# Optimization experiments

Measured on AMD Instinct MI355X. Metric: run time of the kernel, lower is better.

The kernel has to match this reference:

```python
import jax, jax.numpy as jnp
import numpy as np

DELTA = 0.1      # delta from __init__
LN_EPS = 1e-5    # torch LayerNorm default eps

B, IN, OUT, E = 256, 512, 512, 256


def setup_inputs() -> dict:
    key = jax.random.key(0)
    ks = jax.random.split(key, 6)
    return {
        "x": jax.random.normal(ks[0], (B, IN), dtype=jnp.float32),
        # nn.init.normal_(std=0.1), shape (out_features, in_features)
        "weights": 0.1 * jax.random.normal(ks[1], (OUT, IN), dtype=jnp.float32),
        # frozen predicate embeddings (in_features, embedding_dim)
        "pred_emb": jax.random.normal(ks[2], (IN, E), dtype=jnp.float32),
        # nn.Linear(E, OUT): weight (OUT, E), bias (OUT,)
        "attn_w": jax.random.uniform(ks[3], (OUT, E), dtype=jnp.float32,
                                      minval=-1.0, maxval=1.0) / np.sqrt(E),
        "attn_b": jax.random.uniform(ks[4], (OUT,), dtype=jnp.float32,
                                      minval=-1.0, maxval=1.0) / np.sqrt(E),
        # nn.LayerNorm(OUT)
        "ln_g": jnp.ones((OUT,), dtype=jnp.float32),
        "ln_b": jnp.zeros((OUT,), dtype=jnp.float32),
    }


def _layernorm(s, g, b):
    mu = s.mean(axis=-1, keepdims=True)
    var = ((s - mu) ** 2).mean(axis=-1, keepdims=True)
    return (s - mu) * jax.lax.rsqrt(var + LN_EPS) * g + b


def reference(x, weights, pred_emb, attn_w, attn_b, ln_g, ln_b):
    # semantic attention gate: batch-invariant, compute once -> (IN, OUT)
    scores = pred_emb @ attn_w.T + attn_b                    # (IN, OUT)
    sig = jax.nn.sigmoid(_layernorm(scores, ln_g, ln_b))     # (IN, OUT)

    xe = x[:, :, None]                                       # (B, IN, 1)
    wt = weights.T[None]                                     # (1, IN, OUT)
    # abs_weight * attn_adjusted, fused elementwise -> (B, IN, OUT)
    aw = jnp.abs(xe * wt) * (sig[None] * xe)

    bias = aw.max(axis=1) - aw.sum(axis=1)                   # CONJUNCTION: max - sum
    return x @ weights.T + DELTA * bias                      # (B, OUT)
```

## Files before the change

kernel.cpp:

```cpp
#include <hip/hip_runtime.h>
#include <hip/hip_bf16.h>
#include <math.h>

#define B_   256
#define IN_  512
#define OUT_ 512
#define E_   256
#define DELTA_ 0.1f
#define LN_EPS_ 1e-5f

__global__ __launch_bounds__(512)
void k1_scores_ln_sig(const float* __restrict__ pred_emb,
                      const float* __restrict__ attn_w,
                      const float* __restrict__ attn_b,
                      const float* __restrict__ ln_g,
                      const float* __restrict__ ln_b,
                      const float* __restrict__ weights,
                      float2* __restrict__ wv) {
    __shared__ float pe[2][E_];
    __shared__ float red[8][2][2];
    __shared__ float smu[2], srs[2];

    const int t    = threadIdx.x;
    const int lane = t & 63;
    const int wid  = t >> 6;
    const int i0   = blockIdx.x * 2;
    const int o    = t;

    pe[t >> 8][t & 255] = pred_emb[(size_t)(i0 + (t >> 8)) * E_ + (t & 255)];
    __syncthreads();

    const float4* p0 = reinterpret_cast<const float4*>(pe[0]);
    const float4* p1 = reinterpret_cast<const float4*>(pe[1]);
    const float4* wrow = reinterpret_cast<const float4*>(attn_w + (size_t)o * E_);

    float a0 = 0.f, a1 = 0.f;
    #pragma unroll 8
    for (int e4 = 0; e4 < E_ / 4; ++e4) {
        float4 w4 = wrow[e4];
        float4 q0 = p0[e4];
        float4 q1 = p1[e4];
        a0 += q0.x * w4.x + q0.y * w4.y + q0.z * w4.z + q0.w * w4.w;
        a1 += q1.x * w4.x + q1.y * w4.y + q1.z * w4.z + q1.w * w4.w;
    }
    const float bo = attn_b[o];
    a0 += bo;
    a1 += bo;

    {
        float s1 = a0, s2 = a0 * a0;
        float u1 = a1, u2 = a1 * a1;
        #pragma unroll
        for (int off = 32; off > 0; off >>= 1) {
            s1 += __shfl_down(s1, off);
            s2 += __shfl_down(s2, off);
            u1 += __shfl_down(u1, off);
            u2 += __shfl_down(u2, off);
        }
        if (lane == 0) {
            red[wid][0][0] = s1; red[wid][0][1] = s2;
            red[wid][1][0] = u1; red[wid][1][1] = u2;
        }
    }
    __syncthreads();
    if (t < 2) {
        float s1 = 0.f, s2 = 0.f;
        #pragma unroll
        for (int w = 0; w < 8; ++w) { s1 += red[w][t][0]; s2 += red[w][t][1]; }
        float mu  = s1 / (float)OUT_;
        float var = s2 / (float)OUT_ - mu * mu;
        smu[t] = mu;
        srs[t] = rsqrtf(var + LN_EPS_);
    }
    __syncthreads();

    const float g  = ln_g[o];
    const float bb = ln_b[o];
    float z0 = (a0 - smu[0]) * srs[0] * g + bb;
    float z1 = (a1 - smu[1]) * srs[1] * g + bb;
    float sg0 = 1.f / (1.f + expf(-z0));
    float sg1 = 1.f / (1.f + expf(-z1));

    float2 w01 = *reinterpret_cast<const float2*>(weights + (size_t)o * IN_ + i0);
    wv[(size_t)(i0 + 0) * OUT_ + o] = make_float2(w01.x, fabsf(w01.x) * sg0);
    wv[(size_t)(i0 + 1) * OUT_ + o] = make_float2(w01.y, fabsf(w01.y) * sg1);
}

#define K2_SK 4
#define K2_CH 128
#define K2_BO (B_ * OUT_)

__global__ __launch_bounds__(256)
void k2_partials(const float* __restrict__ x,
                 const float2* __restrict__ wv,
                 float* __restrict__ plin,
                 float* __restrict__ pmax) {
    __shared__ float4 xs4[64 * 33];
    __shared__ float2 ws2[K2_CH * 17];

    const int t  = threadIdx.x;
    const int ot = t & 15;
    const int bl = t >> 4;
    const int o0 = blockIdx.x * 16;
    const int b0 = blockIdx.y * 64;
    const int sk = blockIdx.z;
    const int i0 = sk * K2_CH;

    #pragma unroll
    for (int k = 0; k < 8; ++k) {
        int p    = t + k * 256;
        int row  = p >> 5;
        int col4 = p & 31;
        xs4[row * 33 + col4] = reinterpret_cast<const float4*>(
            x + (size_t)(b0 + row) * IN_ + i0)[col4];
    }
    #pragma unroll
    for (int k = 0; k < 8; ++k) {
        int r = bl + 16 * k;
        ws2[r * 17 + ot] = wv[(size_t)(i0 + r) * OUT_ + o0 + ot];
    }
    __syncthreads();

    const int o = o0 + ot;
    float d0 = 0.f, s0 = 0.f, m0 = -INFINITY;
    float d1 = 0.f, s1 = 0.f, m1 = -INFINITY;
    float d2 = 0.f, s2 = 0.f, m2 = -INFINITY;
    float d3 = 0.f, s3 = 0.f, m3 = -INFINITY;

    #pragma unroll 2
    for (int i4 = 0; i4 < K2_CH / 4; ++i4) {
        float4 x0 = xs4[(bl +  0) * 33 + i4];
        float4 x1 = xs4[(bl + 16) * 33 + i4];
        float4 x2 = xs4[(bl + 32) * 33 + i4];
        float4 x3 = xs4[(bl + 48) * 33 + i4];
        float2 w0 = ws2[(4 * i4 + 0) * 17 + ot];
        float2 w1 = ws2[(4 * i4 + 1) * 17 + ot];
        float2 w2 = ws2[(4 * i4 + 2) * 17 + ot];
        float2 w3 = ws2[(4 * i4 + 3) * 17 + ot];
        float p;
        float4 u0 = make_float4(x0.x * fabsf(x0.x), x0.y * fabsf(x0.y),
                                x0.z * fabsf(x0.z), x0.w * fabsf(x0.w));
        float4 u1 = make_float4(x1.x * fabsf(x1.x), x1.y * fabsf(x1.y),
                                x1.z * fabsf(x1.z), x1.w * fabsf(x1.w));
        float4 u2 = make_float4(x2.x * fabsf(x2.x), x2.y * fabsf(x2.y),
                                x2.z * fabsf(x2.z), x2.w * fabsf(x2.w));
        float4 u3 = make_float4(x3.x * fabsf(x3.x), x3.y * fabsf(x3.y),
                                x3.z * fabsf(x3.z), x3.w * fabsf(x3.w));

        d0 = fmaf(x0.x, w0.x, d0); p = u0.x * w0.y; s0 += p; m0 = fmaxf(m0, p);
        d1 = fmaf(x1.x, w0.x, d1); p = u1.x * w0.y; s1 += p; m1 = fmaxf(m1, p);
        d2 = fmaf(x2.x, w0.x, d2); p = u2.x * w0.y; s2 += p; m2 = fmaxf(m2, p);
        d3 = fmaf(x3.x, w0.x, d3); p = u3.x * w0.y; s3 += p; m3 = fmaxf(m3, p);

        d0 = fmaf(x0.y, w1.x, d0); p = u0.y * w1.y; s0 += p; m0 = fmaxf(m0, p);
        d1 = fmaf(x1.y, w1.x, d1); p = u1.y * w1.y; s1 += p; m1 = fmaxf(m1, p);
        d2 = fmaf(x2.y, w1.x, d2); p = u2.y * w1.y; s2 += p; m2 = fmaxf(m2, p);
        d3 = fmaf(x3.y, w1.x, d3); p = u3.y * w1.y; s3 += p; m3 = fmaxf(m3, p);

        d0 = fmaf(x0.z, w2.x, d0); p = u0.z * w2.y; s0 += p; m0 = fmaxf(m0, p);
        d1 = fmaf(x1.z, w2.x, d1); p = u1.z * w2.y; s1 += p; m1 = fmaxf(m1, p);
        d2 = fmaf(x2.z, w2.x, d2); p = u2.z * w2.y; s2 += p; m2 = fmaxf(m2, p);
        d3 = fmaf(x3.z, w2.x, d3); p = u3.z * w2.y; s3 += p; m3 = fmaxf(m3, p);

        d0 = fmaf(x0.w, w3.x, d0); p = u0.w * w3.y; s0 += p; m0 = fmaxf(m0, p);
        d1 = fmaf(x1.w, w3.x, d1); p = u1.w * w3.y; s1 += p; m1 = fmaxf(m1, p);
        d2 = fmaf(x2.w, w3.x, d2); p = u2.w * w3.y; s2 += p; m2 = fmaxf(m2, p);
        d3 = fmaf(x3.w, w3.x, d3); p = u3.w * w3.y; s3 += p; m3 = fmaxf(m3, p);
    }

    const size_t base = (size_t)sk * K2_BO + (size_t)b0 * OUT_ + o;
    plin[base + (size_t)(bl +  0) * OUT_] = d0 - DELTA_ * s0;
    plin[base + (size_t)(bl + 16) * OUT_] = d1 - DELTA_ * s1;
    plin[base + (size_t)(bl + 32) * OUT_] = d2 - DELTA_ * s2;
    plin[base + (size_t)(bl + 48) * OUT_] = d3 - DELTA_ * s3;
    pmax[base + (size_t)(bl +  0) * OUT_] = m0;
    pmax[base + (size_t)(bl + 16) * OUT_] = m1;
    pmax[base + (size_t)(bl + 32) * OUT_] = m2;
    pmax[base + (size_t)(bl + 48) * OUT_] = m3;
}

__global__ __launch_bounds__(256)
void k3_combine(const float4* __restrict__ plin4,
                const float4* __restrict__ pmax4,
                float4* __restrict__ out4) {
    const int g = blockIdx.x * 256 + threadIdx.x;
    const int Q = K2_BO / 4;
    float4 l0 = plin4[g], l1 = plin4[Q + g], l2 = plin4[2 * Q + g], l3 = plin4[3 * Q + g];
    float4 m0 = pmax4[g], m1 = pmax4[Q + g], m2 = pmax4[2 * Q + g], m3 = pmax4[3 * Q + g];
    float4 r;
    r.x = (l0.x + l1.x + l2.x + l3.x) + DELTA_ * fmaxf(fmaxf(m0.x, m1.x), fmaxf(m2.x, m3.x));
    r.y = (l0.y + l1.y + l2.y + l3.y) + DELTA_ * fmaxf(fmaxf(m0.y, m1.y), fmaxf(m2.y, m3.y));
    r.z = (l0.z + l1.z + l2.z + l3.z) + DELTA_ * fmaxf(fmaxf(m0.z, m1.z), fmaxf(m2.z, m3.z));
    r.w = (l0.w + l1.w + l2.w + l3.w) + DELTA_ * fmaxf(fmaxf(m0.w, m1.w), fmaxf(m2.w, m3.w));
    out4[g] = r;
}

extern "C" void kernel_launch(void* const* d_in, const int* in_sizes, int n_in,
                              void* d_out, int out_size, void* d_ws, size_t ws_size,
                              hipStream_t stream) {
    const float* x        = (const float*)d_in[0];
    const float* weights  = (const float*)d_in[1];
    const float* pred_emb = (const float*)d_in[2];
    const float* attn_w   = (const float*)d_in[3];
    const float* attn_b   = (const float*)d_in[4];
    const float* ln_g     = (const float*)d_in[5];
    const float* ln_b     = (const float*)d_in[6];

    float2* wv   = (float2*)d_ws;
    float*  plin = (float*)d_ws + 2 * (size_t)IN_ * OUT_;
    float*  pmax = plin + (size_t)K2_SK * K2_BO;

    k1_scores_ln_sig<<<IN_ / 2, 512, 0, stream>>>(
        pred_emb, attn_w, attn_b, ln_g, ln_b, weights, wv);

    k2_partials<<<dim3(OUT_ / 16, B_ / 64, K2_SK), 256, 0, stream>>>(
        x, wv, plin, pmax);

    k3_combine<<<K2_BO / 4 / 256, 256, 0, stream>>>(
        (const float4*)plin, (const float4*)pmax, (float4*)d_out);
}
```

Baseline: 99.47 us.

## Use 4x4 register tiles in partials kernel with split W/V arrays

The interleaved float2 weight/gate array is split into two planar arrays, with DELTA folded into the gate values so the combine step adds the max directly. The partials kernel now computes a 4-batch by 4-output register tile per thread from float4 shared-memory loads, with 64 outputs per block and split-K raised from 4 to 8 chunks of 64. The gate kernel handles four input rows per block. The aim is more arithmetic per shared-memory load and vectorised stores, at the cost of more registers and double the partial-buffer traffic in the combine kernel.

```diff
diff --git a/kernel.cpp b/kernel.cpp
--- a/kernel.cpp
+++ b/kernel.cpp
@@ -1,5 +1,4 @@
 #include <hip/hip_runtime.h>
-#include <hip/hip_bf16.h>
 #include <math.h>
 
 #define B_   256
@@ -16,54 +15,68 @@
                       const float* __restrict__ ln_g,
                       const float* __restrict__ ln_b,
                       const float* __restrict__ weights,
-                      float2* __restrict__ wv) {
-    __shared__ float pe[2][E_];
-    __shared__ float red[8][2][2];
-    __shared__ float smu[2], srs[2];
+                      float* __restrict__ wA,
+                      float* __restrict__ vA) {
+    __shared__ float pe[4][E_];
+    __shared__ float red[8][4][2];
+    __shared__ float smu[4], srs[4];
 
     const int t    = threadIdx.x;
     const int lane = t & 63;
     const int wid  = t >> 6;
-    const int i0   = blockIdx.x * 2;
+    const int i0   = blockIdx.x * 4;
     const int o    = t;
 
-    pe[t >> 8][t & 255] = pred_emb[(size_t)(i0 + (t >> 8)) * E_ + (t & 255)];
+    #pragma unroll
+    for (int k = 0; k < 2; ++k) {
+        int p = t + 512 * k;
+        pe[p >> 8][p & 255] = pred_emb[(size_t)(i0 + (p >> 8)) * E_ + (p & 255)];
+    }
     __syncthreads();
 
     const float4* p0 = reinterpret_cast<const float4*>(pe[0]);
     const float4* p1 = reinterpret_cast<const float4*>(pe[1]);
+    const float4* p2 = reinterpret_cast<const float4*>(pe[2]);
+    const float4* p3 = reinterpret_cast<const float4*>(pe[3]);
     const float4* wrow = reinterpret_cast<const float4*>(attn_w + (size_t)o * E_);
 
-    float a0 = 0.f, a1 = 0.f;
+    float a0 = 0.f, a1 = 0.f, a2 = 0.f, a3 = 0.f;
     #pragma unroll 8
     for (int e4 = 0; e4 < E_ / 4; ++e4) {
         float4 w4 = wrow[e4];
         float4 q0 = p0[e4];
         float4 q1 = p1[e4];
+        float4 q2 = p2[e4];
+        float4 q3 = p3[e4];
         a0 += q0.x * w4.x + q0.y * w4.y + q0.z * w4.z + q0.w * w4.w;
         a1 += q1.x * w4.x + q1.y * w4.y + q1.z * w4.z + q1.w * w4.w;
+        a2 += q2.x * w4.x + q2.y * w4.y + q2.z * w4.z + q2.w * w4.w;
+        a3 += q3.x * w4.x + q3.y * w4.y + q3.z * w4.z + q3.w * w4.w;
     }
     const float bo = attn_b[o];
-    a0 += bo;
-    a1 += bo;
+    a0 += bo; a1 += bo; a2 += bo; a3 += bo;
 
     {
-        float s1 = a0, s2 = a0 * a0;
-        float u1 = a1, u2 = a1 * a1;
+        float s10 = a0, s20 = a0 * a0;
+        float s11 = a1, s21 = a1 * a1;
+        float s12 = a2, s22 = a2 * a2;
+        float s13 = a3, s23 = a3 * a3;
         #pragma unroll
         for (int off = 32; off > 0; off >>= 1) {
-            s1 += __shfl_down(s1, off);
-            s2 += __shfl_down(s2, off);
-            u1 += __shfl_down(u1, off);
-            u2 += __shfl_down(u2, off);
+            s10 += __shfl_down(s10, off); s20 += __shfl_down(s20, off);
+            s11 += __shfl_down(s11, off); s21 += __shfl_down(s21, off);
+            s12 += __shfl_down(s12, off); s22 += __shfl_down(s22, off);
+            s13 += __shfl_down(s13, off); s23 += __shfl_down(s23, off);
         }
         if (lane == 0) {
-            red[wid][0][0] = s1; red[wid][0][1] = s2;
-            red[wid][1][0] = u1; red[wid][1][1] = u2;
-        }
-    }
-    __syncthreads();
-    if (t < 2) {
+            red[wid][0][0] = s10; red[wid][0][1] = s20;
+            red[wid][1][0] = s11; red[wid][1][1] = s21;
+            red[wid][2][0] = s12; red[wid][2][1] = s22;
+            red[wid][3][0] = s13; red[wid][3][1] = s23;
+        }
+    }
+    __syncthreads();
+    if (t < 4) {
         float s1 = 0.f, s2 = 0.f;
         #pragma unroll
         for (int w = 0; w < 8; ++w) { s1 += red[w][t][0]; s2 += red[w][t][1]; }
@@ -78,105 +91,111 @@
     const float bb = ln_b[o];
     float z0 = (a0 - smu[0]) * srs[0] * g + bb;
     float z1 = (a1 - smu[1]) * srs[1] * g + bb;
+    float z2 = (a2 - smu[2]) * srs[2] * g + bb;
+    float z3 = (a3 - smu[3]) * srs[3] * g + bb;
     float sg0 = 1.f / (1.f + expf(-z0));
     float sg1 = 1.f / (1.f + expf(-z1));
-
-    float2 w01 = *reinterpret_cast<const float2*>(weights + (size_t)o * IN_ + i0);
-    wv[(size_t)(i0 + 0) * OUT_ + o] = make_float2(w01.x, fabsf(w01.x) * sg0);
-    wv[(size_t)(i0 + 1) * OUT_ + o] = make_float2(w01.y, fabsf(w01.y) * sg1);
-}
-
-#define K2_SK 4
-#define K2_CH 128
+    float sg2 = 1.f / (1.f + expf(-z2));
+    float sg3 = 1.f / (1.f + expf(-z3));
+
+    float4 w4 = *reinterpret_cast<const float4*>(weights + (size_t)o * IN_ + i0);
+    wA[(size_t)(i0 + 0) * OUT_ + o] = w4.x;
+    wA[(size_t)(i0 + 1) * OUT_ + o] = w4.y;
+    wA[(size_t)(i0 + 2) * OUT_ + o] = w4.z;
+    wA[(size_t)(i0 + 3) * OUT_ + o] = w4.w;
+    vA[(size_t)(i0 + 0) * OUT_ + o] = DELTA_ * fabsf(w4.x) * sg0;
+    vA[(size_t)(i0 + 1) * OUT_ + o] = DELTA_ * fabsf(w4.y) * sg1;
+    vA[(size_t)(i0 + 2) * OUT_ + o] = DELTA_ * fabsf(w4.z) * sg2;
+    vA[(size_t)(i0 + 3) * OUT_ + o] = DELTA_ * fabsf(w4.w) * sg3;
+}
+
+#define K2_SK 8
+#define K2_CH 64
 #define K2_BO (B_ * OUT_)
 
 __global__ __launch_bounds__(256)
 void k2_partials(const float* __restrict__ x,
-                 const float2* __restrict__ wv,
+                 const float* __restrict__ wA,
+                 const float* __restrict__ vA,
                  float* __restrict__ plin,
                  float* __restrict__ pmax) {
-    __shared__ float4 xs4[64 * 33];
-    __shared__ float2 ws2[K2_CH * 17];
+    __shared__ float4 xs [64 * 17];
+    __shared__ float4 wss[64 * 17];
+    __shared__ float4 vss[64 * 17];
 
     const int t  = threadIdx.x;
-    const int ot = t & 15;
-    const int bl = t >> 4;
-    const int o0 = blockIdx.x * 16;
+    const int oq = t & 15;
+    const int br = t >> 4;
+    const int o0 = blockIdx.x * 64;
     const int b0 = blockIdx.y * 64;
-    const int sk = blockIdx.z;
-    const int i0 = sk * K2_CH;
-
-    #pragma unroll
-    for (int k = 0; k < 8; ++k) {
-        int p    = t + k * 256;
-        int row  = p >> 5;
-        int col4 = p & 31;
-        xs4[row * 33 + col4] = reinterpret_cast<const float4*>(
-            x + (size_t)(b0 + row) * IN_ + i0)[col4];
-    }
-    #pragma unroll
-    for (int k = 0; k < 8; ++k) {
-        int r = bl + 16 * k;
-        ws2[r * 17 + ot] = wv[(size_t)(i0 + r) * OUT_ + o0 + ot];
-    }
-    __syncthreads();
-
-    const int o = o0 + ot;
-    float d0 = 0.f, s0 = 0.f, m0 = -INFINITY;
-    float d1 = 0.f, s1 = 0.f, m1 = -INFINITY;
-    float d2 = 0.f, s2 = 0.f, m2 = -INFINITY;
-    float d3 = 0.f, s3 = 0.f, m3 = -INFINITY;
+    const int i0 = blockIdx.z * K2_CH;
+
+    #pragma unroll
+    for (int k = 0; k < 4; ++k) {
+        int p   = t + k * 256;
+        int row = p >> 4;
+        int c4  = p & 15;
+        xs [row * 17 + c4] = *reinterpret_cast<const float4*>(
+            x  + (size_t)(b0 + row) * IN_  + i0 + c4 * 4);
+        wss[row * 17 + c4] = *reinterpret_cast<const float4*>(
+            wA + (size_t)(i0 + row) * OUT_ + o0 + c4 * 4);
+        vss[row * 17 + c4] = *reinterpret_cast<const float4*>(
+            vA + (size_t)(i0 + row) * OUT_ + o0 + c4 * 4);
+    }
+    __syncthreads();
+
+    float d[4][4], s[4][4], m[4][4];
+    #pragma unroll
+    for (int b = 0; b < 4; ++b)
+        #pragma unroll
+        for (int oo = 0; oo < 4; ++oo) {
+            d[b][oo] = 0.f; s[b][oo] = 0.f; m[b][oo] = -INFINITY;
+        }
 
     #pragma unroll 2
     for (int i4 = 0; i4 < K2_CH / 4; ++i4) {
-        float4 x0 = xs4[(bl +  0) * 33 + i4];
-        float4 x1 = xs4[(bl + 16) * 33 + i4];
-        float4 x2 = xs4[(bl + 32) * 33 + i4];
-        float4 x3 = xs4[(bl + 48) * 33 + i4];
-        float2 w0 = ws2[(4 * i4 + 0) * 17 + ot];
-        float2 w1 = ws2[(4 * i4 + 1) * 17 + ot];
-        float2 w2 = ws2[(4 * i4 + 2) * 17 + ot];
-        float2 w3 = ws2[(4 * i4 + 3) * 17 + ot];
-        float p;
-        float4 u0 = make_float4(x0.x * fabsf(x0.x), x0.y * fabsf(x0.y),
-                                x0.z * fabsf(x0.z), x0.w * fabsf(x0.w));
-        float4 u1 = make_float4(x1.x * fabsf(x1.x), x1.y * fabsf(x1.y),
-                                x1.z * fabsf(x1.z), x1.w * fabsf(x1.w));
-        float4 u2 = make_float4(x2.x * fabsf(x2.x), x2.y * fabsf(x2.y),
-                                x2.z * fabsf(x2.z), x2.w * fabsf(x2.w));
-        float4 u3 = make_float4(x3.x * fabsf(x3.x), x3.y * fabsf(x3.y),
-                                x3.z * fabsf(x3.z), x3.w * fabsf(x3.w));
-
-        d0 = fmaf(x0.x, w0.x, d0); p = u0.x * w0.y; s0 += p; m0 = fmaxf(m0, p);
-        d1 = fmaf(x1.x, w0.x, d1); p = u1.x * w0.y; s1 += p; m1 = fmaxf(m1, p);
-        d2 = fmaf(x2.x, w0.x, d2); p = u2.x * w0.y; s2 += p; m2 = fmaxf(m2, p);
-        d3 = fmaf(x3.x, w0.x, d3); p = u3.x * w0.y; s3 += p; m3 = fmaxf(m3, p);
-
-        d0 = fmaf(x0.y, w1.x, d0); p = u0.y * w1.y; s0 += p; m0 = fmaxf(m0, p);
-        d1 = fmaf(x1.y, w1.x, d1); p = u1.y * w1.y; s1 += p; m1 = fmaxf(m1, p);
-        d2 = fmaf(x2.y, w1.x, d2); p = u2.y * w1.y; s2 += p; m2 = fmaxf(m2, p);
-        d3 = fmaf(x3.y, w1.x, d3); p = u3.y * w1.y; s3 += p; m3 = fmaxf(m3, p);
-
-        d0 = fmaf(x0.z, w2.x, d0); p = u0.z * w2.y; s0 += p; m0 = fmaxf(m0, p);
-        d1 = fmaf(x1.z, w2.x, d1); p = u1.z * w2.y; s1 += p; m1 = fmaxf(m1, p);
-        d2 = fmaf(x2.z, w2.x, d2); p = u2.z * w2.y; s2 += p; m2 = fmaxf(m2, p);
-        d3 = fmaf(x3.z, w2.x, d3); p = u3.z * w2.y; s3 += p; m3 = fmaxf(m3, p);
-
-        d0 = fmaf(x0.w, w3.x, d0); p = u0.w * w3.y; s0 += p; m0 = fmaxf(m0, p);
-        d1 = fmaf(x1.w, w3.x, d1); p = u1.w * w3.y; s1 += p; m1 = fmaxf(m1, p);
-        d2 = fmaf(x2.w, w3.x, d2); p = u2.w * w3.y; s2 += p; m2 = fmaxf(m2, p);
-        d3 = fmaf(x3.w, w3.x, d3); p = u3.w * w3.y; s3 += p; m3 = fmaxf(m3, p);
-    }
-
-    const size_t base = (size_t)sk * K2_BO + (size_t)b0 * OUT_ + o;
-    plin[base + (size_t)(bl +  0) * OUT_] = d0 - DELTA_ * s0;
-    plin[base + (size_t)(bl + 16) * OUT_] = d1 - DELTA_ * s1;
-    plin[base + (size_t)(bl + 32) * OUT_] = d2 - DELTA_ * s2;
-    plin[base + (size_t)(bl + 48) * OUT_] = d3 - DELTA_ * s3;
-    pmax[base + (size_t)(bl +  0) * OUT_] = m0;
-    pmax[base + (size_t)(bl + 16) * OUT_] = m1;
-    pmax[base + (size_t)(bl + 32) * OUT_] = m2;
-    pmax[base + (size_t)(bl + 48) * OUT_] = m3;
+        float4 xv0 = xs[(br +  0) * 17 + i4];
+        float4 xv1 = xs[(br + 16) * 17 + i4];
+        float4 xv2 = xs[(br + 32) * 17 + i4];
+        float4 xv3 = xs[(br + 48) * 17 + i4];
+        float xr[4][4] = {{xv0.x, xv0.y, xv0.z, xv0.w},
+                          {xv1.x, xv1.y, xv1.z, xv1.w},
+                          {xv2.x, xv2.y, xv2.z, xv2.w},
+                          {xv3.x, xv3.y, xv3.z, xv3.w}};
+        float ur[4][4];
+        #pragma unroll
+        for (int b = 0; b < 4; ++b)
+            #pragma unroll
+            for (int ii = 0; ii < 4; ++ii)
+                ur[b][ii] = xr[b][ii] * fabsf(xr[b][ii]);
+
+        #pragma unroll
+        for (int ii = 0; ii < 4; ++ii) {
+            float4 w4 = wss[(i4 * 4 + ii) * 17 + oq];
+            float4 v4 = vss[(i4 * 4 + ii) * 17 + oq];
+            #pragma unroll
+            for (int b = 0; b < 4; ++b) {
+                float xb = xr[b][ii];
+                float ub = ur[b][ii];
+                float p_;
+                d[b][0] = fmaf(xb, w4.x, d[b][0]); p_ = ub * v4.x; s[b][0] += p_; m[b][0] = fmaxf(m[b][0], p_);
+                d[b][1] = fmaf(xb, w4.y, d[b][1]); p_ = ub * v4.y; s[b][1] += p_; m[b][1] = fmaxf(m[b][1], p_);
+                d[b][2] = fmaf(xb, w4.z, d[b][2]); p_ = ub * v4.z; s[b][2] += p_; m[b][2] = fmaxf(m[b][2], p_);
+                d[b][3] = fmaf(xb, w4.w, d[b][3]); p_ = ub * v4.w; s[b][3] += p_; m[b][3] = fmaxf(m[b][3], p_);
+            }
+        }
+    }
+
+    #pragma unroll
+    for (int b = 0; b < 4; ++b) {
+        const int row = b0 + br + 16 * b;
+        const size_t idx = ((size_t)blockIdx.z * B_ + row) * OUT_ + o0 + oq * 4;
+        *reinterpret_cast<float4*>(plin + idx) =
+            make_float4(d[b][0] - s[b][0], d[b][1] - s[b][1],
+                        d[b][2] - s[b][2], d[b][3] - s[b][3]);
+        *reinterpret_cast<float4*>(pmax + idx) =
+            make_float4(m[b][0], m[b][1], m[b][2], m[b][3]);
+    }
 }
 
 __global__ __launch_bounds__(256)
@@ -185,14 +204,17 @@
                 float4* __restrict__ out4) {
     const int g = blockIdx.x * 256 + threadIdx.x;
     const int Q = K2_BO / 4;
-    float4 l0 = plin4[g], l1 = plin4[Q + g], l2 = plin4[2 * Q + g], l3 = plin4[3 * Q + g];
-    float4 m0 = pmax4[g], m1 = pmax4[Q + g], m2 = pmax4[2 * Q + g], m3 = pmax4[3 * Q + g];
-    float4 r;
-    r.x = (l0.x + l1.x + l2.x + l3.x) + DELTA_ * fmaxf(fmaxf(m0.x, m1.x), fmaxf(m2.x, m3.x));
-    r.y = (l0.y + l1.y + l2.y + l3.y) + DELTA_ * fmaxf(fmaxf(m0.y, m1.y), fmaxf(m2.y, m3.y));
-    r.z = (l0.z + l1.z + l2.z + l3.z) + DELTA_ * fmaxf(fmaxf(m0.z, m1.z), fmaxf(m2.z, m3.z));
-    r.w = (l0.w + l1.w + l2.w + l3.w) + DELTA_ * fmaxf(fmaxf(m0.w, m1.w), fmaxf(m2.w, m3.w));
-    out4[g] = r;
+    float4 l  = plin4[g];
+    float4 mx = pmax4[g];
+    #pragma unroll
+    for (int p = 1; p < K2_SK; ++p) {
+        float4 lp = plin4[(size_t)p * Q + g];
+        float4 mp = pmax4[(size_t)p * Q + g];
+        l.x += lp.x; l.y += lp.y; l.z += lp.z; l.w += lp.w;
+        mx.x = fmaxf(mx.x, mp.x); mx.y = fmaxf(mx.y, mp.y);
+        mx.z = fmaxf(mx.z, mp.z); mx.w = fmaxf(mx.w, mp.w);
+    }
+    out4[g] = make_float4(l.x + mx.x, l.y + mx.y, l.z + mx.z, l.w + mx.w);
 }
 
 extern "C" void kernel_launch(void* const* d_in, const int* in_sizes, int n_in,
@@ -206,15 +228,16 @@
     const float* ln_g     = (const float*)d_in[5];
     const float* ln_b     = (const float*)d_in[6];
 
-    float2* wv   = (float2*)d_ws;
-    float*  plin = (float*)d_ws + 2 * (size_t)IN_ * OUT_;
-    float*  pmax = plin + (size_t)K2_SK * K2_BO;
-
-    k1_scores_ln_sig<<<IN_ / 2, 512, 0, stream>>>(
-        pred_emb, attn_w, attn_b, ln_g, ln_b, weights, wv);
-
-    k2_partials<<<dim3(OUT_ / 16, B_ / 64, K2_SK), 256, 0, stream>>>(
-        x, wv, plin, pmax);
+    float* wA   = (float*)d_ws;
+    float* vA   = wA + (size_t)IN_ * OUT_;
+    float* plin = vA + (size_t)IN_ * OUT_;
+    float* pmax = plin + (size_t)K2_SK * K2_BO;
+
+    k1_scores_ln_sig<<<IN_ / 4, 512, 0, stream>>>(
+        pred_emb, attn_w, attn_b, ln_g, ln_b, weights, wA, vA);
+
+    k2_partials<<<dim3(OUT_ / 64, B_ / 64, K2_SK), 256, 0, stream>>>(
+        x, wA, vA, plin, pmax);
 
     k3_combine<<<K2_BO / 4 / 256, 256, 0, stream>>>(
         (const float4*)plin, (const float4*)pmax, (float4*)d_out);
```

Result: no change. 99.68 us (+0.2%).
